# Optimization experiments

Measured on AMD Instinct MI355X. Metric: run time of the kernel, lower is better.

## Reference

```python
import jax, jax.numpy as jnp
import numpy as np

N = 20000      # nodes
E = 320000     # edges (before self-loops)
F_IN = 50      # PPI num_features
C1 = 256       # per-head channels, conv1/conv2
H1 = 4         # heads, conv1/conv2
C3 = 121       # PPI num_classes, conv3 per-head channels
H3 = 6         # heads, conv3 (concat=False -> mean)


def gat_conv(x, src, dst, W, a_src, a_dst, b, heads, ch, concat, n):
    """PyG-style GATConv with self-loops already included in (src, dst).
    Messages flow src -> dst; softmax is over incoming edges of each dst node."""
    h = (x @ W).reshape(n, heads, ch)                      # [N, H, C]
    es = jnp.sum(h * a_src, axis=-1)                       # [N, H]
    ed = jnp.sum(h * a_dst, axis=-1)                       # [N, H]
    e = jax.nn.leaky_relu(es[src] + ed[dst], 0.2)          # [E', H]
    m = jax.ops.segment_max(e, dst, num_segments=n)        # stable softmax per dst
    e = jnp.exp(e - m[dst])
    denom = jax.ops.segment_sum(e, dst, num_segments=n)
    alpha = e / jnp.maximum(denom[dst], 1e-16)             # [E', H]
    out = jax.ops.segment_sum(alpha[:, :, None] * h[src], dst, num_segments=n)  # [N, H, C]
    out = out.reshape(n, heads * ch) if concat else out.mean(axis=1)
    return out + b


def setup_inputs() -> dict:
    key = jax.random.key(0)
    ks = jax.random.split(key, 16)

    def p(k, shape, fan_in):
        return (jax.random.normal(k, shape, jnp.float32) / np.float32(np.sqrt(fan_in)))

    x = jax.random.normal(ks[0], (N, F_IN), jnp.float32)
    edge_index = jax.random.randint(ks[1], (2, E), 0, N, dtype=jnp.int64)
    D1 = H1 * C1  # 1024
    return dict(
        x=x, edge_index=edge_index,
        W1=p(ks[2], (F_IN, D1), F_IN), a1s=p(ks[3], (H1, C1), C1), a1d=p(ks[4], (H1, C1), C1), b1=jnp.zeros((D1,), jnp.float32),
        Wl1=p(ks[5], (F_IN, D1), F_IN), bl1=jnp.zeros((D1,), jnp.float32),
        W2=p(ks[6], (D1, D1), D1), a2s=p(ks[7], (H1, C1), C1), a2d=p(ks[8], (H1, C1), C1), b2=jnp.zeros((D1,), jnp.float32),
        Wl2=p(ks[9], (D1, D1), D1), bl2=jnp.zeros((D1,), jnp.float32),
        W3=p(ks[10], (D1, H3 * C3), D1), a3s=p(ks[11], (H3, C3), C3), a3d=p(ks[12], (H3, C3), C3), b3=jnp.zeros((C3,), jnp.float32),
        Wl3=p(ks[13], (D1, C3), D1), bl3=jnp.zeros((C3,), jnp.float32),
    )


def reference(x, edge_index, W1, a1s, a1d, b1, Wl1, bl1, W2, a2s, a2d, b2, Wl2, bl2, W3, a3s, a3d, b3, Wl3, bl3):
    n = x.shape[0]
    loop = jnp.arange(n, dtype=edge_index.dtype)           # PyG GATConv adds self-loops
    src = jnp.concatenate([edge_index[0], loop])
    dst = jnp.concatenate([edge_index[1], loop])
    x1 = jax.nn.elu(gat_conv(x, src, dst, W1, a1s, a1d, b1, H1, C1, True, n) + x @ Wl1 + bl1)
    x2 = jax.nn.elu(gat_conv(x1, src, dst, W2, a2s, a2d, b2, H1, C1, True, n) + x1 @ Wl2 + bl2)
    out = gat_conv(x2, src, dst, W3, a3s, a3d, b3, H3, C3, False, n) + x2 @ Wl3 + bl3
    return out
```

## Files before the change

### kernel.cpp

```cpp
#include <hip/hip_runtime.h>
#include <hip/hip_bf16.h>
#include <math.h>

typedef __bf16 bf16;
typedef __attribute__((ext_vector_type(4))) __bf16 bf16x4;
typedef __attribute__((ext_vector_type(8))) __bf16 bf16x8;
typedef __attribute__((ext_vector_type(4))) float f32x4;

#define N_NODES 20000
#define N_EDGES 320000
#define E2 (N_EDGES + N_NODES)
#define F_IN 50
#define D1 1024
#define NP12 2048
#define NP3 896
#define SG 2048
#define KA 320

#define PO_A1S 0
#define PO_A1D 1024
#define PO_B1  2048
#define PO_BL1 3072
#define PO_A2S 4096
#define PO_A2D 5120
#define PO_B2  6144
#define PO_BL2 7168
#define PO_A3S 8192
#define PO_A3D 8918
#define PO_B3  9644
#define PO_BL3 9765
#define PO_END 9886

#define PB_PADX  5000
#define PB_WF1   1280
#define PB_PAR   39
#define PB_LOG1  5000

__device__ __forceinline__ int clampi(int v, int lo, int hi)
{
    return v < lo ? lo : (v > hi ? hi : v);
}

__device__ __forceinline__ float loadf(const void* p, long idx, int isb)
{
    return isb ? (float)((const bf16*)p)[idx] : ((const float*)p)[idx];
}

__device__ __forceinline__ int loadei(const int* ei, long idx, int i64)
{
    return i64 ? ei[2 * idx] : ei[idx];
}

__global__ void k_detect(const int* __restrict__ ei,
                         const unsigned short* __restrict__ xw,
                         int* __restrict__ flags)
{
    if (blockIdx.x != 0 || threadIdx.x != 0) return;
    int allz = 1;
    for (int i = 0; i < 128; ++i)
        if (ei[2 * i + 1] != 0) { allz = 0; break; }
    int inr = 0;
    for (int i = 0; i < 128; ++i) {
        int e = (xw[2 * i] >> 7) & 0xFF;
        if (e >= 100 && e <= 140) inr++;
    }
    flags[0] = allz;
    flags[1] = (inr >= 64) ? 1 : 0;
}

template <bool BACT>
__global__ __launch_bounds__(256) void k_gemm(const bf16* __restrict__ A,
                                              const bf16* __restrict__ Bt,
                                              bf16* __restrict__ C,
                                              int M, int K, int lda, int ldb, int ldc,
                                              int mtiles, int ntiles,
                                              const bf16* __restrict__ bias)
{
    __shared__ bf16 As[128 * 64];
    __shared__ bf16 Bs[128 * 64];

    int id = blockIdx.x;
    int gfull = mtiles >> 3;
    int base  = gfull * 8 * ntiles;
    int x, y;
    if (id < base) {
        int gsz = 8 * ntiles;
        int g = id / gsz;
        int r = id - g * gsz;
        x = g * 8 + (r & 7);
        y = r >> 3;
    } else {
        int rem = mtiles - (gfull << 3);
        int r = id - base;
        x = (gfull << 3) + r % rem;
        y = r / rem;
    }
    const int m0 = x * 128;
    const int n0 = y * 128;

    const int tid  = threadIdx.x;
    const int wave = tid >> 6;
    const int lane = tid & 63;
    const int wm   = (wave >> 1) * 64;
    const int wn   = (wave & 1) * 64;
    const int frow  = lane & 15;

    const int srow = wave * 32 + (lane >> 3);
    const int scol = (((lane & 7) ^ (lane >> 3)) * 8);

    f32x4 acc[4][4];
#pragma unroll
    for (int i = 0; i < 4; ++i)
#pragma unroll
        for (int j = 0; j < 4; ++j)
#pragma unroll
            for (int r = 0; r < 4; ++r) acc[i][j][r] = 0.f;

    for (int k0 = 0; k0 < K; k0 += 64) {
#pragma unroll
        for (int i = 0; i < 4; ++i) {
            int ra = srow + i * 8;
            int ga = m0 + ra; if (ga > M - 1) ga = M - 1;
            __builtin_amdgcn_global_load_lds(
                (const __attribute__((address_space(1))) void*)(A + (size_t)ga * lda + k0 + scol),
                (__attribute__((address_space(3))) void*)(As + wave * 2048 + i * 512),
                16, 0, 0);
            int gb = n0 + ra;
            __builtin_amdgcn_global_load_lds(
                (const __attribute__((address_space(1))) void*)(Bt + (size_t)gb * ldb + k0 + scol),
                (__attribute__((address_space(3))) void*)(Bs + wave * 2048 + i * 512),
                16, 0, 0);
        }
        __syncthreads();
#pragma unroll
        for (int kk = 0; kk < 2; ++kk) {
            const int coff = (((kk * 4 + (lane >> 4)) ^ (frow & 7)) << 3);
            bf16x8 af[4], bfr[4];
#pragma unroll
            for (int i = 0; i < 4; ++i) {
                af[i]  = *(const bf16x8*)(As + (wm + i * 16 + frow) * 64 + coff);
                bfr[i] = *(const bf16x8*)(Bs + (wn + i * 16 + frow) * 64 + coff);
            }
#pragma unroll
            for (int i = 0; i < 4; ++i)
#pragma unroll
                for (int j = 0; j < 4; ++j)
                    acc[i][j] = __builtin_amdgcn_mfma_f32_16x16x32_bf16(af[i], bfr[j], acc[i][j], 0, 0, 0);
        }
        __syncthreads();
    }

#pragma unroll
    for (int i = 0; i < 4; ++i) {
#pragma unroll
        for (int j = 0; j < 4; ++j) {
            int rbase = m0 + wm + i * 16 + (lane >> 4) * 4;
            int col   = n0 + wn + j * 16 + frow;
            if constexpr (BACT) {
                float bv = (float)bias[col];
#pragma unroll
                for (int r = 0; r < 4; ++r) {
                    int row = rbase + r;
                    if (row < M) {
                        float v = acc[i][j][r] + bv;
                        v = (v > 0.f) ? v : (__expf(v) - 1.f);
                        C[(size_t)row * ldc + col] = (bf16)v;
                    }
                }
            } else {
#pragma unroll
                for (int r = 0; r < 4; ++r) {
                    int row = rbase + r;
                    if (row < M) C[(size_t)row * ldc + col] = (bf16)acc[i][j][r];
                }
            }
        }
    }
}

__global__ __launch_bounds__(256) void k_veca(const void* __restrict__ W1,
                                              const void* __restrict__ a1s,
                                              const void* __restrict__ a1d,
                                              const void* __restrict__ b1,
                                              const void* __restrict__ bl1,
                                              float* __restrict__ ws, float* __restrict__ wd,
                                              bf16* __restrict__ bsum,
                                              const int* __restrict__ flags)
{
    const int isb = flags[1];
    const int k = blockIdx.x;
    const int h = threadIdx.x >> 6;
    const int c0 = threadIdx.x & 63;
    float s = 0.f, d = 0.f;
    if (k < F_IN) {
        for (int c = c0; c < 256; c += 64) {
            float wv = loadf(W1, (long)k * D1 + h * 256 + c, isb);
            s += wv * loadf(a1s, h * 256 + c, isb);
            d += wv * loadf(a1d, h * 256 + c, isb);
        }
    }
#pragma unroll
    for (int off = 32; off; off >>= 1) {
        s += __shfl_xor(s, off);
        d += __shfl_xor(d, off);
    }
    if (c0 == 0) { ws[k * 4 + h] = s; wd[k * 4 + h] = d; }
    if (k < 4) {
        int j = k * 256 + threadIdx.x;
        bsum[j] = (bf16)(loadf(b1, j, isb) + loadf(bl1, j, isb));
    }
}

struct P12 { const void* s[12]; };

__global__ __launch_bounds__(256) void k_prep(const void* __restrict__ x,
                                              const void* __restrict__ W1,
                                              const void* __restrict__ Wl1,
                                              P12 ps,
                                              bf16* __restrict__ A2,
                                              bf16* __restrict__ Bt,
                                              bf16* __restrict__ pool,
                                              const float* __restrict__ ws,
                                              const float* __restrict__ wd,
                                              float* __restrict__ es,
                                              float* __restrict__ ed,
                                              const int* __restrict__ flags)
{
    const int isb = flags[1];
    int b = blockIdx.x;

    if (b < PB_PADX) {
        int idx = b * 256 + threadIdx.x;
        int n = idx >> 6, k = idx & 63;
        A2[(size_t)n * KA + 256 + k] = (k < F_IN) ? (bf16)loadf(x, (long)n * F_IN + k, isb)
                                                  : (bf16)0.f;
        return;
    }
    b -= PB_PADX;

    if (b < PB_WF1) {
        int idx = b * 256 + threadIdx.x;
        int j = idx / KA;
        int kp = idx - j * KA;
        float v = 0.f;
        if (kp < 256) {
            int hp = kp >> 6, k = kp & 63;
            if ((j >> 8) == hp && k < F_IN) v = loadf(W1, (long)k * D1 + j, isb);
        } else {
            int k = kp - 256;
            if (k < F_IN) v = loadf(Wl1, (long)k * D1 + j, isb);
        }
        Bt[idx] = (bf16)v;
        return;
    }
    b -= PB_WF1;

    if (b < PB_PAR) {
        const int off[13] = {PO_A1S, PO_A1D, PO_B1, PO_BL1, PO_A2S, PO_A2D, PO_B2,
                             PO_BL2, PO_A3S, PO_A3D, PO_B3, PO_BL3, PO_END};
        int idx = b * 256 + threadIdx.x;
        if (idx < PO_END) {
            int seg = 0;
            while (idx >= off[seg + 1]) seg++;
            pool[idx] = (bf16)loadf(ps.s[seg], idx - off[seg], isb);
        }
        return;
    }
    b -= PB_PAR;

    const int wave = threadIdx.x >> 6;
    const int lane = threadIdx.x & 63;
    const int n = b * 4 + wave;
    if (n >= N_NODES) return;
    float xv = (lane < F_IN) ? loadf(x, (long)n * F_IN + lane, isb) : 0.f;
    f32x4 wsv = *(const f32x4*)(ws + lane * 4);
    f32x4 wdv = *(const f32x4*)(wd + lane * 4);
    float s[4], d[4];
#pragma unroll
    for (int h = 0; h < 4; ++h) { s[h] = xv * wsv[h]; d[h] = xv * wdv[h]; }
#pragma unroll
    for (int off = 32; off; off >>= 1)
#pragma unroll
        for (int h = 0; h < 4; ++h) {
            s[h] += __shfl_xor(s[h], off);
            d[h] += __shfl_xor(d[h], off);
        }
    if (lane == 0) {
#pragma unroll
        for (int h = 0; h < 4; ++h) { es[n * 4 + h] = s[h]; ed[n * 4 + h] = d[h]; }
    }
}

__global__ __launch_bounds__(256) void k_wcatT(const void* __restrict__ Wa,
                                               const void* __restrict__ Wb,
                                               bf16* __restrict__ Bt,
                                               int split, int da, int db,
                                               const int* __restrict__ flags)
{
    __shared__ bf16 T[64][65];
    const int isb = flags[1];
    const int k0 = blockIdx.x * 64;
    const int n0 = blockIdx.y * 64;
    const int r = threadIdx.x >> 6;
    const int c = threadIdx.x & 63;
    const int n = n0 + c;
#pragma unroll
    for (int kk = 0; kk < 16; ++kk) {
        int k = k0 + r + kk * 4;
        float v = 0.f;
        if (n < split)           v = loadf(Wa, (long)k * da + n, isb);
        else if (n < split + db) v = loadf(Wb, (long)k * db + (n - split), isb);
        T[r + kk * 4][c] = (bf16)v;
    }
    __syncthreads();
#pragma unroll
    for (int kk = 0; kk < 16; ++kk) {
        int nn = r + kk * 4;
        Bt[(size_t)(n0 + nn) * 1024 + k0 + c] = T[c][nn];
    }
}

__global__ void k_count(const int* __restrict__ ei, int* __restrict__ cnt,
                        const int* __restrict__ flags)
{
    int e = blockIdx.x * 256 + threadIdx.x;
    if (e >= E2) return;
    int i64 = flags[0];
    int d = (e < N_EDGES) ? loadei(ei, (long)N_EDGES + e, i64) : (e - N_EDGES);
    d = clampi(d, 0, N_NODES - 1);
    atomicAdd(&cnt[d], 1);
}

__global__ __launch_bounds__(256) void k_scan(const int* __restrict__ cnt,
                                              int* __restrict__ rp,
                                              int* __restrict__ cur)
{
    __shared__ int ssum[256];
    int tid = threadIdx.x;
    const int chunk = (N_NODES + 255) / 256;
    int lo = tid * chunk;
    int hi = lo + chunk; if (hi > N_NODES) hi = N_NODES;
    int s = 0;
    for (int i = lo; i < hi; ++i) s += cnt[i];
    ssum[tid] = s;
    __syncthreads();
    if (tid == 0) {
        int run = 0;
        for (int i = 0; i < 256; ++i) { int t = ssum[i]; ssum[i] = run; run += t; }
        rp[N_NODES] = run;
    }
    __syncthreads();
    int run = ssum[tid];
    for (int i = lo; i < hi; ++i) { rp[i] = run; cur[i] = run; run += cnt[i]; }
}

__global__ void k_fill(const int* __restrict__ ei, int* __restrict__ cur,
                       int* __restrict__ ss, const int* __restrict__ flags)
{
    int e = blockIdx.x * 256 + threadIdx.x;
    if (e >= E2) return;
    int i64 = flags[0];
    int s, d;
    if (e < N_EDGES) {
        s = loadei(ei, e, i64);
        d = loadei(ei, (long)N_EDGES + e, i64);
    } else {
        s = e - N_EDGES; d = s;
    }
    s = clampi(s, 0, N_NODES - 1);
    d = clampi(d, 0, N_NODES - 1);
    int pos = atomicAdd(&cur[d], 1);
    if (pos >= 0 && pos < E2) ss[pos] = s;
}

__global__ __launch_bounds__(256) void k_aggx(bf16* __restrict__ A2,
                                              const float* __restrict__ es,
                                              const float* __restrict__ ed,
                                              const int* __restrict__ rp,
                                              const int* __restrict__ ss)
{
    __shared__ float smx[4], sinv[4], sed[4];
    __shared__ float sal[64 * 4];
    __shared__ int   ssrc[64];

    const int n   = blockIdx.x;
    const int tid = threadIdx.x;
    int r0 = clampi(rp[n], 0, E2);
    int r1 = clampi(rp[n + 1], r0, E2);
    const int deg = r1 - r0;

    const int sw = tid >> 5, ln = tid & 31;
    if (sw < 4) {
        int h = sw;
        float edn = ed[n * 4 + h];
        float mx = -1e30f;
        for (int e = ln; e < deg; e += 32) {
            int s = clampi(ss[r0 + e], 0, N_NODES - 1);
            float w = es[s * 4 + h] + edn;
            w = (w > 0.f) ? w : 0.2f * w;
            mx = fmaxf(mx, w);
        }
#pragma unroll
        for (int off = 16; off; off >>= 1) mx = fmaxf(mx, __shfl_xor(mx, off, 32));
        float sm = 0.f;
        for (int e = ln; e < deg; e += 32) {
            int s = clampi(ss[r0 + e], 0, N_NODES - 1);
            float w = es[s * 4 + h] + edn;
            w = (w > 0.f) ? w : 0.2f * w;
            sm += __expf(w - mx);
        }
#pragma unroll
        for (int off = 16; off; off >>= 1) sm += __shfl_xor(sm, off, 32);
        if (ln == 0) { smx[h] = mx; sinv[h] = 1.f / fmaxf(sm, 1e-16f); sed[h] = edn; }
    }
    __syncthreads();

    const int k  = tid & 63;
    const int hh = tid >> 6;
    float acc = 0.f;

    for (int e0 = 0; e0 < deg; e0 += 64) {
        int ce = min(64, deg - e0);
        int ce4 = (ce + 3) & ~3;
        __syncthreads();
        if (tid < ce4 * 4) {
            int e = tid >> 2, h = tid & 3;
            int valid = (e < ce);
            int s = valid ? clampi(ss[r0 + e0 + e], 0, N_NODES - 1) : 0;
            float w = es[s * 4 + h] + sed[h];
            w = (w > 0.f) ? w : 0.2f * w;
            sal[e * 4 + h] = valid ? __expf(w - smx[h]) * sinv[h] : 0.f;
            if (h == 0) ssrc[e] = s;
        }
        __syncthreads();
        for (int e = 0; e < ce4; e += 4) {
            float xv[4], al[4];
#pragma unroll
            for (int p = 0; p < 4; ++p) {
                int s = ssrc[e + p];
                xv[p] = (float)A2[(size_t)s * KA + 256 + k];
            }
#pragma unroll
            for (int p = 0; p < 4; ++p) al[p] = sal[(e + p) * 4 + hh];
#pragma unroll
            for (int p = 0; p < 4; ++p) acc += al[p] * xv[p];
        }
    }
    A2[(size_t)n * KA + hh * 64 + k] = (bf16)acc;
}

template <int H, int C>
__global__ __launch_bounds__(256) void k_logits(const bf16* __restrict__ G,
                                                const bf16* __restrict__ as_,
                                                const bf16* __restrict__ ad_,
                                                float* __restrict__ es, float* __restrict__ ed)
{
    const int wave = threadIdx.x >> 6;
    const int lane = threadIdx.x & 63;
    const int n = blockIdx.x * 4 + wave;
    if (n >= N_NODES) return;

#pragma unroll
    for (int h = 0; h < H; ++h) {
        float s = 0.f, d = 0.f;
        if constexpr (C == 256) {
            bf16x4 g  = *(const bf16x4*)(G + (size_t)n * SG + h * 256 + lane * 4);
            bf16x4 av = *(const bf16x4*)(as_ + h * 256 + lane * 4);
            bf16x4 dv = *(const bf16x4*)(ad_ + h * 256 + lane * 4);
#pragma unroll
            for (int j = 0; j < 4; ++j) {
                float gv = (float)g[j];
                s += gv * (float)av[j];
                d += gv * (float)dv[j];
            }
        } else {
            for (int c = lane; c < C; c += 64) {
                float hv = (float)G[(size_t)n * SG + h * C + c];
                s += hv * (float)as_[h * C + c];
                d += hv * (float)ad_[h * C + c];
            }
        }
#pragma unroll
        for (int off = 32; off; off >>= 1) {
            s += __shfl_xor(s, off);
            d += __shfl_xor(d, off);
        }
        if (lane == 0) { es[n * H + h] = s; ed[n * H + h] = d; }
    }
}

__global__ __launch_bounds__(256) void k_aggw(const bf16* __restrict__ G,
                                              const bf16* __restrict__ S,
                                              const float* __restrict__ es,
                                              const float* __restrict__ ed,
                                              const int* __restrict__ rp,
                                              const int* __restrict__ ss,
                                              const bf16* __restrict__ bgat,
                                              const bf16* __restrict__ bskip,
                                              bf16* __restrict__ out, int sout)
{
    __shared__ float sal[4][4][65];
    __shared__ int   ssrc[4][64];

    const int w    = threadIdx.x >> 6;
    const int lane = threadIdx.x & 63;
    const int n    = blockIdx.x * 4 + w;
    if (n >= N_NODES) return;

    int r0 = clampi(rp[n], 0, E2);
    int r1 = clampi(rp[n + 1], r0, E2);
    const int deg = r1 - r0;

    f32x4 edn = *(const f32x4*)(ed + n * 4);

    float mx[4] = {-1e30f, -1e30f, -1e30f, -1e30f};
    float sm[4] = {0.f, 0.f, 0.f, 0.f};
    for (int c0 = 0; c0 < deg; c0 += 64) {
        const int e = c0 + lane;
        const bool val = (e < deg);
        const int s = val ? clampi(ss[r0 + e], 0, N_NODES - 1) : 0;
        f32x4 esv = *(const f32x4*)(es + s * 4);
        float w4[4], mc[4];
#pragma unroll
        for (int h = 0; h < 4; ++h) {
            float v = esv[h] + edn[h];
            v = (v > 0.f) ? v : 0.2f * v;
            w4[h] = val ? v : -1e30f;
            mc[h] = w4[h];
        }
#pragma unroll
        for (int off = 32; off; off >>= 1)
#pragma unroll
            for (int h = 0; h < 4; ++h) mc[h] = fmaxf(mc[h], __shfl_xor(mc[h], off));
        float ps[4];
#pragma unroll
        for (int h = 0; h < 4; ++h) {
            float mn = fmaxf(mx[h], mc[h]);
            float f  = __expf(mx[h] - mn);
            ps[h] = __expf(w4[h] - mn);
            mx[h] = mn;
            sm[h] *= f;
        }
#pragma unroll
        for (int off = 32; off; off >>= 1)
#pragma unroll
            for (int h = 0; h < 4; ++h) ps[h] += __shfl_xor(ps[h], off);
#pragma unroll
        for (int h = 0; h < 4; ++h) sm[h] += ps[h];
    }
    float sinv[4];
#pragma unroll
    for (int h = 0; h < 4; ++h) sinv[h] = 1.f / fmaxf(sm[h], 1e-16f);

    const int myh  = lane >> 4;
    const int c0ch = lane * 16;
    float acc[16];
#pragma unroll
    for (int j = 0; j < 16; ++j) acc[j] = 0.f;

    for (int c0 = 0; c0 < deg; c0 += 64) {
        const int ce = min(64, deg - c0);
        const bool val = (lane < ce);
        const int e = c0 + lane;
        const int s = val ? clampi(ss[r0 + e], 0, N_NODES - 1) : 0;
        f32x4 esv = *(const f32x4*)(es + s * 4);
#pragma unroll
        for (int h = 0; h < 4; ++h) {
            float v = esv[h] + edn[h];
            v = (v > 0.f) ? v : 0.2f * v;
            sal[w][h][lane] = val ? __expf(v - mx[h]) * sinv[h] : 0.f;
        }
        ssrc[w][lane] = s;
        const int ce4 = (ce + 3) & ~3;
        for (int eb = 0; eb < ce4; eb += 4) {
            int sg[4]; float a[4];
#pragma unroll
            for (int p = 0; p < 4; ++p) {
                sg[p] = ssrc[w][eb + p];
                a[p]  = sal[w][myh][eb + p];
            }
            bf16x8 g0[4], g1[4];
#pragma unroll
            for (int p = 0; p < 4; ++p) {
                const bf16* gp = G + (size_t)sg[p] * SG + c0ch;
                g0[p] = *(const bf16x8*)gp;
                g1[p] = *(const bf16x8*)(gp + 8);
            }
#pragma unroll
            for (int p = 0; p < 4; ++p) {
#pragma unroll
                for (int j = 0; j < 8; ++j) acc[j]     += a[p] * (float)g0[p][j];
#pragma unroll
                for (int j = 0; j < 8; ++j) acc[j + 8] += a[p] * (float)g1[p][j];
            }
        }
    }

    bf16x8 bg0 = *(const bf16x8*)(bgat + c0ch);
    bf16x8 bg1 = *(const bf16x8*)(bgat + c0ch + 8);
    bf16x8 sk0 = *(const bf16x8*)(S + (size_t)n * SG + c0ch);
    bf16x8 sk1 = *(const bf16x8*)(S + (size_t)n * SG + c0ch + 8);
    bf16x8 bs0 = *(const bf16x8*)(bskip + c0ch);
    bf16x8 bs1 = *(const bf16x8*)(bskip + c0ch + 8);
    bf16x8 ov0, ov1;
#pragma unroll
    for (int j = 0; j < 8; ++j) {
        float v = acc[j] + (float)bg0[j] + (float)sk0[j] + (float)bs0[j];
        v = (v > 0.f) ? v : (__expf(v) - 1.f);
        ov0[j] = (bf16)v;
        float u = acc[j + 8] + (float)bg1[j] + (float)sk1[j] + (float)bs1[j];
        u = (u > 0.f) ? u : (__expf(u) - 1.f);
        ov1[j] = (bf16)u;
    }
    *(bf16x8*)(out + (size_t)n * sout + c0ch)     = ov0;
    *(bf16x8*)(out + (size_t)n * sout + c0ch + 8) = ov1;
}

template <int H, int C, bool MEAN, bool ELU, bool EXTOUT>
__global__ __launch_bounds__(256) void k_agg(const bf16* __restrict__ G,
                                             const bf16* __restrict__ S,
                                             const float* __restrict__ es,
                                             const float* __restrict__ ed,
                                             const int* __restrict__ rp,
                                             const int* __restrict__ ss,
                                             const bf16* __restrict__ bgat,
                                             const bf16* __restrict__ bskip,
                                             void* __restrict__ out, int sout,
                                             const int* __restrict__ flags)
{
    constexpr int D  = H * C;
    constexpr int NV = (D + 3) / 4;
    constexpr int CH = 256;
    __shared__ float smx[H], sinv[H], sed[H];
    __shared__ float sal[CH * H];
    __shared__ int   ssrc[CH];

    const int n   = blockIdx.x;
    const int tid = threadIdx.x;
    int r0 = clampi(rp[n], 0, E2);
    int r1 = clampi(rp[n + 1], r0, E2);
    const int deg = r1 - r0;

    const int sw = tid >> 5, ln = tid & 31;
    for (int h = sw; h < H; h += 8) {
        float edn = ed[n * H + h];
        float mx = -1e30f;
        for (int e = ln; e < deg; e += 32) {
            int s = clampi(ss[r0 + e], 0, N_NODES - 1);
            float w = es[s * H + h] + edn;
            w = (w > 0.f) ? w : 0.2f * w;
            mx = fmaxf(mx, w);
        }
#pragma unroll
        for (int off = 16; off; off >>= 1) mx = fmaxf(mx, __shfl_xor(mx, off, 32));
        float sm = 0.f;
        for (int e = ln; e < deg; e += 32) {
            int s = clampi(ss[r0 + e], 0, N_NODES - 1);
            float w = es[s * H + h] + edn;
            w = (w > 0.f) ? w : 0.2f * w;
            sm += __expf(w - mx);
        }
#pragma unroll
        for (int off = 16; off; off >>= 1) sm += __shfl_xor(sm, off, 32);
        if (ln == 0) { smx[h] = mx; sinv[h] = 1.f / fmaxf(sm, 1e-16f); sed[h] = edn; }
    }
    __syncthreads();

    const int c0 = tid * 4;
    const int hA = (c0 < D) ? (c0 / C) : 0;
    const int hB = (c0 + 3 < D) ? ((c0 + 3) / C) : hA;
    int hj1 = ((c0 + 1 < D) ? ((c0 + 1) / C) : hA) == hA;
    int hj2 = ((c0 + 2 < D) ? ((c0 + 2) / C) : hA) == hA;
    const bool active = (tid < NV);

    float acc[4] = {0.f, 0.f, 0.f, 0.f};

    for (int e0 = 0; e0 < deg; e0 += CH) {
        int ce = min(CH, deg - e0);
        int ce4 = (ce + 3) & ~3;
        __syncthreads();
        for (int t = tid; t < ce4 * H; t += 256) {
            int e = t / H, h = t - e * H;
            int valid = (e < ce);
            int s = valid ? clampi(ss[r0 + e0 + e], 0, N_NODES - 1) : 0;
            float w = es[s * H + h] + sed[h];
            w = (w > 0.f) ? w : 0.2f * w;
            sal[e * H + h] = valid ? __expf(w - smx[h]) * sinv[h] : 0.f;
            if (h == 0) ssrc[e] = s;
        }
        __syncthreads();
        if (active) {
            for (int eb = 0; eb < ce4; eb += 4) {
                int sg[4];
#pragma unroll
                for (int p = 0; p < 4; ++p) sg[p] = ssrc[eb + p];
                bf16x4 g[4];
#pragma unroll
                for (int p = 0; p < 4; ++p)
                    g[p] = *(const bf16x4*)(G + (size_t)sg[p] * SG + c0);
                if constexpr (C % 4 == 0) {
                    float a[4];
#pragma unroll
                    for (int p = 0; p < 4; ++p) a[p] = sal[(eb + p) * H + hA];
#pragma unroll
                    for (int p = 0; p < 4; ++p)
#pragma unroll
                        for (int j = 0; j < 4; ++j)
                            acc[j] += a[p] * (float)g[p][j];
                } else {
#pragma unroll
                    for (int p = 0; p < 4; ++p) {
                        float aL = sal[(eb + p) * H + hA];
                        float aH = sal[(eb + p) * H + hB];
                        acc[0] += aL * (float)g[p][0];
                        acc[1] += (hj1 ? aL : aH) * (float)g[p][1];
                        acc[2] += (hj2 ? aL : aH) * (float)g[p][2];
                        acc[3] += aH * (float)g[p][3];
                    }
                }
            }
        }
    }

    const int outbf = EXTOUT ? flags[1] : 1;

    if constexpr (!MEAN) {
        if (active) {
            bf16x4 bg = *(const bf16x4*)(bgat + c0);
            bf16x4 sk = *(const bf16x4*)(S + (size_t)n * SG + c0);
            bf16x4 bs = *(const bf16x4*)(bskip + c0);
            bf16x4 ov;
#pragma unroll
            for (int j = 0; j < 4; ++j) {
                float v = acc[j] + (float)bg[j] + (float)sk[j] + (float)bs[j];
                if (ELU) v = (v > 0.f) ? v : (__expf(v) - 1.f);
                ov[j] = (bf16)v;
            }
            *(bf16x4*)((bf16*)out + (size_t)n * sout + c0) = ov;
        }
    } else {
        __shared__ float sagg[D];
        if (active) {
#pragma unroll
            for (int j = 0; j < 4; ++j) {
                int c = c0 + j;
                if (c < D) sagg[c] = acc[j];
            }
        }
        __syncthreads();
        for (int c = tid; c < C; c += 256) {
            float v = 0.f;
#pragma unroll
            for (int h = 0; h < H; ++h) v += sagg[h * C + c];
            v *= (1.f / H);
            v += (float)bgat[c] + (float)S[(size_t)n * SG + c] + (float)bskip[c];
            if (outbf) ((bf16*)out)[(size_t)n * sout + c] = (bf16)v;
            else       ((float*)out)[(size_t)n * sout + c] = v;
        }
    }
}

extern "C" void kernel_launch(void* const* d_in, const int* in_sizes, int n_in,
                              void* d_out, int out_size, void* d_ws, size_t ws_size,
                              hipStream_t stream)
{
    const void* x   = d_in[0];
    const int*  ei  = (const int*)d_in[1];
    const void* W1  = d_in[2];
    const void* Wl1 = d_in[6];
    const void* W2  = d_in[8];
    const void* Wl2 = d_in[12];
    const void* W3  = d_in[14];
    const void* Wl3 = d_in[18];

    P12 ps;
    ps.s[0] = d_in[3];  ps.s[1] = d_in[4];  ps.s[2] = d_in[5];  ps.s[3] = d_in[7];
    ps.s[4] = d_in[9];  ps.s[5] = d_in[10]; ps.s[6] = d_in[11]; ps.s[7] = d_in[13];
    ps.s[8] = d_in[15]; ps.s[9] = d_in[16]; ps.s[10] = d_in[17]; ps.s[11] = d_in[19];

    char* w = (char*)d_ws;
    auto alloc = [&](size_t bytes) {
        char* p = w;
        w += (bytes + 255) & ~(size_t)255;
        return p;
    };
    int*   flags = (int*)alloc(64);
    int*   cnt   = (int*)alloc((size_t)N_NODES * 4);
    int*   rp    = (int*)alloc((size_t)(N_NODES + 1) * 4);
    int*   cur   = (int*)alloc((size_t)N_NODES * 4);
    int*   ss    = (int*)alloc((size_t)E2 * 4);
    float* es    = (float*)alloc((size_t)N_NODES * 6 * 4);
    float* ed    = (float*)alloc((size_t)N_NODES * 6 * 4);
    bf16*  pool  = (bf16*)alloc((size_t)PO_END * 2);
    float* ws1   = (float*)alloc((size_t)64 * 4 * 4);
    float* wd1   = (float*)alloc((size_t)64 * 4 * 4);
    bf16*  bsum  = (bf16*)alloc((size_t)D1 * 2);
    bf16*  Bt    = (bf16*)alloc((size_t)NP12 * 1024 * 2);
    bf16*  X     = (bf16*)alloc((size_t)N_NODES * D1 * 2);
    bf16*  WS    = (bf16*)alloc((size_t)N_NODES * SG * 2);
    bf16*  A2    = WS;

    k_detect<<<1, 64, 0, stream>>>(ei, (const unsigned short*)x, flags);

    hipMemsetAsync(cnt, 0, N_NODES * 4, stream);
    k_count<<<(E2 + 255) / 256, 256, 0, stream>>>(ei, cnt, flags);
    k_scan<<<1, 256, 0, stream>>>(cnt, rp, cur);
    k_fill<<<(E2 + 255) / 256, 256, 0, stream>>>(ei, cur, ss, flags);

    const dim3 blk(256);
    const int MT = (N_NODES + 127) / 128;

    k_veca<<<64, 256, 0, stream>>>(W1, ps.s[0], ps.s[1], ps.s[2], ps.s[3],
                                   ws1, wd1, bsum, flags);
    k_prep<<<PB_PADX + PB_WF1 + PB_PAR + PB_LOG1, 256, 0, stream>>>(
        x, W1, Wl1, ps, A2, Bt, pool, ws1, wd1, es, ed, flags);
    k_aggx<<<N_NODES, 256, 0, stream>>>(A2, es, ed, rp, ss);
    k_gemm<true><<<MT * (D1 / 128), blk, 0, stream>>>(A2, Bt, X, N_NODES, KA, KA, KA, D1,
                                                      MT, D1 / 128, bsum);

    k_wcatT<<<dim3(16, NP12 / 64), blk, 0, stream>>>(W2, Wl2, Bt, 1024, 1024, 1024, flags);
    k_gemm<false><<<MT * (NP12 / 128), blk, 0, stream>>>(X, Bt, WS, N_NODES, 1024, 1024, 1024, SG,
                                                         MT, NP12 / 128, nullptr);
    k_logits<4, 256><<<N_NODES / 4, 256, 0, stream>>>(WS, pool + PO_A2S, pool + PO_A2D, es, ed);
    k_aggw<<<N_NODES / 4, 256, 0, stream>>>(
        WS, WS + D1, es, ed, rp, ss, pool + PO_B2, pool + PO_BL2, X, D1);

    k_wcatT<<<dim3(16, NP3 / 64), blk, 0, stream>>>(W3, Wl3, Bt, 726, 726, 121, flags);
    k_gemm<false><<<MT * (NP3 / 128), blk, 0, stream>>>(X, Bt, WS, N_NODES, 1024, 1024, 1024, SG,
                                                        MT, NP3 / 128, nullptr);
    k_logits<6, 121><<<N_NODES / 4, 256, 0, stream>>>(WS, pool + PO_A3S, pool + PO_A3D, es, ed);
    k_agg<6, 121, true, false, true><<<N_NODES, 256, 0, stream>>>(
        WS, WS + 726, es, ed, rp, ss, pool + PO_B3, pool + PO_BL3, d_out, 121, flags);
}
```

Measured before the change: 648.4 us.

## Switch layer-1 and layer-3 aggregation kernels to one wavefront per node

Replaces the block-per-node aggregation kernels for the first (input-space) and final GAT layers with wave-per-node kernels that process four nodes per block. Softmax max and sum are computed in a single online pass using wave shuffles instead of two passes with block syncs. The gather is restructured so lanes load wider vectors (8 or 12 bf16), followed by a shuffle or shared-memory fold. This removes __syncthreads and idle threads for low-degree nodes, at the cost of more registers per lane and serial per-wave work on high-degree nodes.

```diff
diff --git a/kernel.cpp b/kernel.cpp
--- a/kernel.cpp
+++ b/kernel.cpp
@@ -373,80 +373,118 @@
     if (pos >= 0 && pos < E2) ss[pos] = s;
 }
 
-__global__ __launch_bounds__(256) void k_aggx(bf16* __restrict__ A2,
-                                              const float* __restrict__ es,
-                                              const float* __restrict__ ed,
-                                              const int* __restrict__ rp,
-                                              const int* __restrict__ ss)
-{
-    __shared__ float smx[4], sinv[4], sed[4];
-    __shared__ float sal[64 * 4];
-    __shared__ int   ssrc[64];
-
-    const int n   = blockIdx.x;
-    const int tid = threadIdx.x;
+__global__ __launch_bounds__(256) void k_aggxw(bf16* __restrict__ A2,
+                                               const float* __restrict__ es,
+                                               const float* __restrict__ ed,
+                                               const int* __restrict__ rp,
+                                               const int* __restrict__ ss)
+{
+    __shared__ float sal[4][4][65];
+    __shared__ int   ssrc[4][64];
+
+    const int w    = threadIdx.x >> 6;
+    const int lane = threadIdx.x & 63;
+    const int n    = blockIdx.x * 4 + w;
+    if (n >= N_NODES) return;
+
     int r0 = clampi(rp[n], 0, E2);
     int r1 = clampi(rp[n + 1], r0, E2);
     const int deg = r1 - r0;
 
-    const int sw = tid >> 5, ln = tid & 31;
-    if (sw < 4) {
-        int h = sw;
-        float edn = ed[n * 4 + h];
-        float mx = -1e30f;
-        for (int e = ln; e < deg; e += 32) {
-            int s = clampi(ss[r0 + e], 0, N_NODES - 1);
-            float w = es[s * 4 + h] + edn;
-            w = (w > 0.f) ? w : 0.2f * w;
-            mx = fmaxf(mx, w);
-        }
-#pragma unroll
-        for (int off = 16; off; off >>= 1) mx = fmaxf(mx, __shfl_xor(mx, off, 32));
-        float sm = 0.f;
-        for (int e = ln; e < deg; e += 32) {
-            int s = clampi(ss[r0 + e], 0, N_NODES - 1);
-            float w = es[s * 4 + h] + edn;
-            w = (w > 0.f) ? w : 0.2f * w;
-            sm += __expf(w - mx);
-        }
-#pragma unroll
-        for (int off = 16; off; off >>= 1) sm += __shfl_xor(sm, off, 32);
-        if (ln == 0) { smx[h] = mx; sinv[h] = 1.f / fmaxf(sm, 1e-16f); sed[h] = edn; }
-    }
-    __syncthreads();
-
-    const int k  = tid & 63;
-    const int hh = tid >> 6;
-    float acc = 0.f;
-
-    for (int e0 = 0; e0 < deg; e0 += 64) {
-        int ce = min(64, deg - e0);
-        int ce4 = (ce + 3) & ~3;
-        __syncthreads();
-        if (tid < ce4 * 4) {
-            int e = tid >> 2, h = tid & 3;
-            int valid = (e < ce);
-            int s = valid ? clampi(ss[r0 + e0 + e], 0, N_NODES - 1) : 0;
-            float w = es[s * 4 + h] + sed[h];
-            w = (w > 0.f) ? w : 0.2f * w;
-            sal[e * 4 + h] = valid ? __expf(w - smx[h]) * sinv[h] : 0.f;
-            if (h == 0) ssrc[e] = s;
-        }
-        __syncthreads();
-        for (int e = 0; e < ce4; e += 4) {
-            float xv[4], al[4];
-#pragma unroll
-            for (int p = 0; p < 4; ++p) {
-                int s = ssrc[e + p];
-                xv[p] = (float)A2[(size_t)s * KA + 256 + k];
-            }
-#pragma unroll
-            for (int p = 0; p < 4; ++p) al[p] = sal[(e + p) * 4 + hh];
-#pragma unroll
-            for (int p = 0; p < 4; ++p) acc += al[p] * xv[p];
-        }
-    }
-    A2[(size_t)n * KA + hh * 64 + k] = (bf16)acc;
+    f32x4 edn = *(const f32x4*)(ed + n * 4);
+
+    float mx[4] = {-1e30f, -1e30f, -1e30f, -1e30f};
+    float sm[4] = {0.f, 0.f, 0.f, 0.f};
+    for (int c0 = 0; c0 < deg; c0 += 64) {
+        const int e = c0 + lane;
+        const bool val = (e < deg);
+        const int s = val ? clampi(ss[r0 + e], 0, N_NODES - 1) : 0;
+        f32x4 esv = *(const f32x4*)(es + s * 4);
+        float w4[4], mc[4];
+#pragma unroll
+        for (int h = 0; h < 4; ++h) {
+            float v = esv[h] + edn[h];
+            v = (v > 0.f) ? v : 0.2f * v;
+            w4[h] = val ? v : -1e30f;
+            mc[h] = w4[h];
+        }
+#pragma unroll
+        for (int off = 32; off; off >>= 1)
+#pragma unroll
+            for (int h = 0; h < 4; ++h) mc[h] = fmaxf(mc[h], __shfl_xor(mc[h], off));
+        float ps[4];
+#pragma unroll
+        for (int h = 0; h < 4; ++h) {
+            float mn = fmaxf(mx[h], mc[h]);
+            float f  = __expf(mx[h] - mn);
+            ps[h] = __expf(w4[h] - mn);
+            mx[h] = mn;
+            sm[h] *= f;
+        }
+#pragma unroll
+        for (int off = 32; off; off >>= 1)
+#pragma unroll
+            for (int h = 0; h < 4; ++h) ps[h] += __shfl_xor(ps[h], off);
+#pragma unroll
+        for (int h = 0; h < 4; ++h) sm[h] += ps[h];
+    }
+    float sinv[4];
+#pragma unroll
+    for (int h = 0; h < 4; ++h) sinv[h] = 1.f / fmaxf(sm[h], 1e-16f);
+
+    const int g  = lane >> 3;
+    const int cb = (lane & 7) * 8;
+    float acc[4][8];
+#pragma unroll
+    for (int h = 0; h < 4; ++h)
+#pragma unroll
+        for (int j = 0; j < 8; ++j) acc[h][j] = 0.f;
+
+    for (int c0 = 0; c0 < deg; c0 += 64) {
+        const int ce = min(64, deg - c0);
+        const bool val = (lane < ce);
+        const int e = c0 + lane;
+        const int s = val ? clampi(ss[r0 + e], 0, N_NODES - 1) : 0;
+        f32x4 esv = *(const f32x4*)(es + s * 4);
+#pragma unroll
+        for (int h = 0; h < 4; ++h) {
+            float v = esv[h] + edn[h];
+            v = (v > 0.f) ? v : 0.2f * v;
+            sal[w][h][lane] = val ? __expf(v - mx[h]) * sinv[h] : 0.f;
+        }
+        ssrc[w][lane] = s;
+        const int ce8 = (ce + 7) & ~7;
+        for (int eb = 0; eb < ce8; eb += 8) {
+            const int sg = ssrc[w][eb + g];
+            bf16x8 xv = *(const bf16x8*)(A2 + (size_t)sg * KA + 256 + cb);
+            float a[4];
+#pragma unroll
+            for (int h = 0; h < 4; ++h) a[h] = sal[w][h][eb + g];
+#pragma unroll
+            for (int h = 0; h < 4; ++h)
+#pragma unroll
+                for (int j = 0; j < 8; ++j) acc[h][j] += a[h] * (float)xv[j];
+        }
+    }
+
+#pragma unroll
+    for (int off = 8; off <= 32; off <<= 1)
+#pragma unroll
+        for (int h = 0; h < 4; ++h)
+#pragma unroll
+            for (int j = 0; j < 8; ++j) acc[h][j] += __shfl_xor(acc[h][j], off);
+
+    if (g < 4) {
+        bf16x8 ov;
+#pragma unroll
+        for (int j = 0; j < 8; ++j) {
+            float v = (g == 0) ? acc[0][j]
+                    : (g == 1) ? acc[1][j]
+                    : (g == 2) ? acc[2][j] : acc[3][j];
+            ov[j] = (bf16)v;
+        }
+        *(bf16x8*)(A2 + (size_t)n * KA + g * 64 + cb) = ov;
+    }
 }
 
 template <int H, int C>
@@ -616,147 +654,137 @@
     *(bf16x8*)(out + (size_t)n * sout + c0ch + 8) = ov1;
 }
 
-template <int H, int C, bool MEAN, bool ELU, bool EXTOUT>
-__global__ __launch_bounds__(256) void k_agg(const bf16* __restrict__ G,
-                                             const bf16* __restrict__ S,
-                                             const float* __restrict__ es,
-                                             const float* __restrict__ ed,
-                                             const int* __restrict__ rp,
-                                             const int* __restrict__ ss,
-                                             const bf16* __restrict__ bgat,
-                                             const bf16* __restrict__ bskip,
-                                             void* __restrict__ out, int sout,
-                                             const int* __restrict__ flags)
-{
-    constexpr int D  = H * C;
-    constexpr int NV = (D + 3) / 4;
-    constexpr int CH = 256;
-    __shared__ float smx[H], sinv[H], sed[H];
-    __shared__ float sal[CH * H];
-    __shared__ int   ssrc[CH];
-
-    const int n   = blockIdx.x;
-    const int tid = threadIdx.x;
+__global__ __launch_bounds__(256) void k_aggw3(const bf16* __restrict__ G,
+                                               const bf16* __restrict__ S,
+                                               const float* __restrict__ es,
+                                               const float* __restrict__ ed,
+                                               const int* __restrict__ rp,
+                                               const int* __restrict__ ss,
+                                               const bf16* __restrict__ bgat,
+                                               const bf16* __restrict__ bskip,
+                                               void* __restrict__ out, int sout,
+                                               const int* __restrict__ flags)
+{
+    __shared__ float sal[4][6][65];
+    __shared__ int   ssrc[4][64];
+    __shared__ float sfold[4][728];
+
+    const int w    = threadIdx.x >> 6;
+    const int lane = threadIdx.x & 63;
+    const int n    = blockIdx.x * 4 + w;
+    if (n >= N_NODES) return;
+
     int r0 = clampi(rp[n], 0, E2);
     int r1 = clampi(rp[n + 1], r0, E2);
     const int deg = r1 - r0;
 
-    const int sw = tid >> 5, ln = tid & 31;
-    for (int h = sw; h < H; h += 8) {
-        float edn = ed[n * H + h];
-        float mx = -1e30f;
-        for (int e = ln; e < deg; e += 32) {
-            int s = clampi(ss[r0 + e], 0, N_NODES - 1);
-            float w = es[s * H + h] + edn;
-            w = (w > 0.f) ? w : 0.2f * w;
-            mx = fmaxf(mx, w);
-        }
-#pragma unroll
-        for (int off = 16; off; off >>= 1) mx = fmaxf(mx, __shfl_xor(mx, off, 32));
-        float sm = 0.f;
-        for (int e = ln; e < deg; e += 32) {
-            int s = clampi(ss[r0 + e], 0, N_NODES - 1);
-            float w = es[s * H + h] + edn;
-            w = (w > 0.f) ? w : 0.2f * w;
-            sm += __expf(w - mx);
-        }
-#pragma unroll
-        for (int off = 16; off; off >>= 1) sm += __shfl_xor(sm, off, 32);
-        if (ln == 0) { smx[h] = mx; sinv[h] = 1.f / fmaxf(sm, 1e-16f); sed[h] = edn; }
-    }
-    __syncthreads();
-
-    const int c0 = tid * 4;
-    const int hA = (c0 < D) ? (c0 / C) : 0;
-    const int hB = (c0 + 3 < D) ? ((c0 + 3) / C) : hA;
-    int hj1 = ((c0 + 1 < D) ? ((c0 + 1) / C) : hA) == hA;
-    int hj2 = ((c0 + 2 < D) ? ((c0 + 2) / C) : hA) == hA;
-    const bool active = (tid < NV);
-
-    float acc[4] = {0.f, 0.f, 0.f, 0.f};
-
-    for (int e0 = 0; e0 < deg; e0 += CH) {
-        int ce = min(CH, deg - e0);
-        int ce4 = (ce + 3) & ~3;
-        __syncthreads();
-        for (int t = tid; t < ce4 * H; t += 256) {
-            int e = t / H, h = t - e * H;
-            int valid = (e < ce);
-            int s = valid ? clampi(ss[r0 + e0 + e], 0, N_NODES - 1) : 0;
-            float w = es[s * H + h] + sed[h];
-            w = (w > 0.f) ? w : 0.2f * w;
-            sal[e * H + h] = valid ? __expf(w - smx[h]) * sinv[h] : 0.f;
-            if (h == 0) ssrc[e] = s;
-        }
-        __syncthreads();
-        if (active) {
-            for (int eb = 0; eb < ce4; eb += 4) {
-                int sg[4];
-#pragma unroll
-                for (int p = 0; p < 4; ++p) sg[p] = ssrc[eb + p];
-                bf16x4 g[4];
-#pragma unroll
-                for (int p = 0; p < 4; ++p)
-                    g[p] = *(const bf16x4*)(G + (size_t)sg[p] * SG + c0);
-                if constexpr (C % 4 == 0) {
-                    float a[4];
-#pragma unroll
-                    for (int p = 0; p < 4; ++p) a[p] = sal[(eb + p) * H + hA];
-#pragma unroll
-                    for (int p = 0; p < 4; ++p)
-#pragma unroll
-                        for (int j = 0; j < 4; ++j)
-                            acc[j] += a[p] * (float)g[p][j];
-                } else {
-#pragma unroll
-                    for (int p = 0; p < 4; ++p) {
-                        float aL = sal[(eb + p) * H + hA];
-                        float aH = sal[(eb + p) * H + hB];
-                        acc[0] += aL * (float)g[p][0];
-                        acc[1] += (hj1 ? aL : aH) * (float)g[p][1];
-                        acc[2] += (hj2 ? aL : aH) * (float)g[p][2];
-                        acc[3] += aH * (float)g[p][3];
-                    }
-                }
+    float edn[6];
+#pragma unroll
+    for (int h = 0; h < 6; ++h) edn[h] = ed[n * 6 + h];
+
+    float mx[6], sm[6];
+#pragma unroll
+    for (int h = 0; h < 6; ++h) { mx[h] = -1e30f; sm[h] = 0.f; }
+    for (int c0 = 0; c0 < deg; c0 += 64) {
+        const int e = c0 + lane;
+        const bool val = (e < deg);
+        const int s = val ? clampi(ss[r0 + e], 0, N_NODES - 1) : 0;
+        const float* ep = es + (size_t)s * 6;
+        float w6[6], mc[6];
+#pragma unroll
+        for (int h = 0; h < 6; ++h) {
+            float v = ep[h] + edn[h];
+            v = (v > 0.f) ? v : 0.2f * v;
+            w6[h] = val ? v : -1e30f;
+            mc[h] = w6[h];
+        }
+#pragma unroll
+        for (int off = 32; off; off >>= 1)
+#pragma unroll
+            for (int h = 0; h < 6; ++h) mc[h] = fmaxf(mc[h], __shfl_xor(mc[h], off));
+        float ps[6];
+#pragma unroll
+        for (int h = 0; h < 6; ++h) {
+            float mn = fmaxf(mx[h], mc[h]);
+            float f  = __expf(mx[h] - mn);
+            ps[h] = __expf(w6[h] - mn);
+            mx[h] = mn;
+            sm[h] *= f;
+        }
+#pragma unroll
+        for (int off = 32; off; off >>= 1)
+#pragma unroll
+            for (int h = 0; h < 6; ++h) ps[h] += __shfl_xor(ps[h], off);
+#pragma unroll
+        for (int h = 0; h < 6; ++h) sm[h] += ps[h];
+    }
+    float sinv[6];
+#pragma unroll
+    for (int h = 0; h < 6; ++h) sinv[h] = 1.f / fmaxf(sm[h], 1e-16f);
+
+    const int c0ch = lane * 12;
+    const int hA = min(c0ch / 121, 5);
+    const int hB = min((c0ch + 11) / 121, 5);
+    bool jA[12];
+#pragma unroll
+    for (int j = 0; j < 12; ++j) jA[j] = (min((c0ch + j) / 121, 5) == hA);
+
+    float acc[12];
+#pragma unroll
+    for (int j = 0; j < 12; ++j) acc[j] = 0.f;
+
+    for (int c0 = 0; c0 < deg; c0 += 64) {
+        const int ce = min(64, deg - c0);
+        const bool val = (lane < ce);
+        const int e = c0 + lane;
+        const int s = val ? clampi(ss[r0 + e], 0, N_NODES - 1) : 0;
+        const float* ep = es + (size_t)s * 6;
+#pragma unroll
+        for (int h = 0; h < 6; ++h) {
+            float v = ep[h] + edn[h];
+            v = (v > 0.f) ? v : 0.2f * v;
+            sal[w][h][lane] = val ? __expf(v - mx[h]) * sinv[h] : 0.f;
+        }
+        ssrc[w][lane] = s;
+        const int ce4 = (ce + 3) & ~3;
+        for (int eb = 0; eb < ce4; eb += 4) {
+            int sg[4]; float aL[4], aH[4];
+#pragma unroll
+            for (int p = 0; p < 4; ++p) {
+                sg[p] = ssrc[w][eb + p];
+                aL[p] = sal[w][hA][eb + p];
+                aH[p] = sal[w][hB][eb + p];
             }
-        }
-    }
-
-    const int outbf = EXTOUT ? flags[1] : 1;
-
-    if constexpr (!MEAN) {
-        if (active) {
-            bf16x4 bg = *(const bf16x4*)(bgat + c0);
-            bf16x4 sk = *(const bf16x4*)(S + (size_t)n * SG + c0);
-            bf16x4 bs = *(const bf16x4*)(bskip + c0);
-            bf16x4 ov;
-#pragma unroll
-            for (int j = 0; j < 4; ++j) {
-                float v = acc[j] + (float)bg[j] + (float)sk[j] + (float)bs[j];
-                if (ELU) v = (v > 0.f) ? v : (__expf(v) - 1.f);
-                ov[j] = (bf16)v;
+#pragma unroll
+            for (int p = 0; p < 4; ++p) {
+                const bf16* gp = G + (size_t)sg[p] * SG + c0ch;
+                bf16x4 g0 = *(const bf16x4*)gp;
+                bf16x4 g1 = *(const bf16x4*)(gp + 4);
+                bf16x4 g2 = *(const bf16x4*)(gp + 8);
+#pragma unroll
+                for (int j = 0; j < 4; ++j) acc[j]     += (jA[j]     ? aL[p] : aH[p]) * (float)g0[j];
+#pragma unroll
+                for (int j = 0; j < 4; ++j) acc[4 + j] += (jA[4 + j] ? aL[p] : aH[p]) * (float)g1[j];
+#pragma unroll
+                for (int j = 0; j < 4; ++j) acc[8 + j] += (jA[8 + j] ? aL[p] : aH[p]) * (float)g2[j];
             }
-            *(bf16x4*)((bf16*)out + (size_t)n * sout + c0) = ov;
-        }
-    } else {
-        __shared__ float sagg[D];
-        if (active) {
-#pragma unroll
-            for (int j = 0; j < 4; ++j) {
-                int c = c0 + j;
-                if (c < D) sagg[c] = acc[j];
-            }
-        }
-        __syncthreads();
-        for (int c = tid; c < C; c += 256) {
-            float v = 0.f;
-#pragma unroll
-            for (int h = 0; h < H; ++h) v += sagg[h * C + c];
-            v *= (1.f / H);
-            v += (float)bgat[c] + (float)S[(size_t)n * SG + c] + (float)bskip[c];
-            if (outbf) ((bf16*)out)[(size_t)n * sout + c] = (bf16)v;
-            else       ((float*)out)[(size_t)n * sout + c] = v;
-        }
+        }
+    }
+
+#pragma unroll
+    for (int j = 0; j < 12; ++j) {
+        int c = c0ch + j;
+        if (c < 726) sfold[w][c] = acc[j];
+    }
+    const int outbf = flags[1];
+    for (int c = lane; c < 121; c += 64) {
+        float v = 0.f;
+#pragma unroll
+        for (int h = 0; h < 6; ++h) v += sfold[w][h * 121 + c];
+        v *= (1.f / 6.f);
+        v += (float)bgat[c] + (float)S[(size_t)n * SG + c] + (float)bskip[c];
+        if (outbf) ((bf16*)out)[(size_t)n * sout + c] = (bf16)v;
+        else       ((float*)out)[(size_t)n * sout + c] = v;
     }
 }
 
@@ -814,7 +842,7 @@
                                    ws1, wd1, bsum, flags);
     k_prep<<<PB_PADX + PB_WF1 + PB_PAR + PB_LOG1, 256, 0, stream>>>(
         x, W1, Wl1, ps, A2, Bt, pool, ws1, wd1, es, ed, flags);
-    k_aggx<<<N_NODES, 256, 0, stream>>>(A2, es, ed, rp, ss);
+    k_aggxw<<<N_NODES / 4, 256, 0, stream>>>(A2, es, ed, rp, ss);
     k_gemm<true><<<MT * (D1 / 128), blk, 0, stream>>>(A2, Bt, X, N_NODES, KA, KA, KA, D1,
                                                       MT, D1 / 128, bsum);
 
@@ -829,6 +857,6 @@
     k_gemm<false><<<MT * (NP3 / 128), blk, 0, stream>>>(X, Bt, WS, N_NODES, 1024, 1024, 1024, SG,
                                                         MT, NP3 / 128, nullptr);
     k_logits<6, 121><<<N_NODES / 4, 256, 0, stream>>>(WS, pool + PO_A3S, pool + PO_A3D, es, ed);
-    k_agg<6, 121, true, false, true><<<N_NODES, 256, 0, stream>>>(
+    k_aggw3<<<N_NODES / 4, 256, 0, stream>>>(
         WS, WS + 726, es, ed, rp, ss, pool + PO_B3, pool + PO_BL3, d_out, 121, flags);
 }
```

New measurement: 635.0 us. 2.1% less time.
